# Performance work log

Hardware: AMD Instinct MI355X
Metric: run time of the kernel (lower is better)

The kernel has to match this reference:

```python
import jax, jax.numpy as jnp
import numpy as np

GRID_NUM = 5   # number of grid intervals (pykan default)
SPLINE_K = 3   # B-spline degree (pykan default)
GRID_RANGE = (-1.0, 1.0)


def make_grid(in_dim):
    # Extended uniform grid: num + 2k + 1 knots per input dim, shared values.
    h = (GRID_RANGE[1] - GRID_RANGE[0]) / GRID_NUM
    pts = GRID_RANGE[0] + h * jnp.arange(-SPLINE_K, GRID_NUM + SPLINE_K + 1, dtype=jnp.float32)
    return jnp.broadcast_to(pts, (in_dim, pts.shape[0]))  # (in_dim, num+2k+1)


def bspline_basis(x, grid, k):
    # Cox-de Boor recursion. x: (n, d); grid: (d, m). Returns (n, d, m-1-k).
    xe = x[..., None]            # (n, d, 1)
    g = grid[None]               # (1, d, m)
    B = ((xe >= g[..., :-1]) & (xe < g[..., 1:])).astype(x.dtype)
    for p in range(1, k + 1):
        left = (xe - g[..., :-(p + 1)]) / (g[..., p:-1] - g[..., :-(p + 1)])
        right = (g[..., p + 1:] - xe) / (g[..., p + 1:] - g[..., 1:-p])
        B = left * B[..., :-1] + right * B[..., 1:]
    return B


def kan_layer(x, coef, scale_base, scale_sp, grid):
    # x: (n, in); coef: (in, out, G+k); scales: (in, out)
    basis = bspline_basis(x, grid, SPLINE_K)              # (n, in, G+k)
    base = jax.nn.silu(x)                                 # (n, in)
    # y[n,o] = sum_i scale_base[i,o]*silu(x[n,i]) + scale_sp[i,o]*sum_g B[n,i,g]*coef[i,o,g]
    spline = jnp.einsum('nig,iog->no', basis, coef * scale_sp[:, :, None])
    return base @ scale_base + spline


def setup_inputs() -> dict:
    key = jax.random.key(0)
    ks = jax.random.split(key, 5)
    b, s, hid, ffn = 2, 4096, 512, 2048
    nb = GRID_NUM + SPLINE_K  # 8 basis functions
    x = jax.random.normal(ks[0], (b, s, hid), dtype=jnp.float32)
    coef1 = 0.1 * jax.random.normal(ks[1], (hid, ffn, nb), dtype=jnp.float32)
    scale_base1 = (1.0 / np.sqrt(hid)) * jax.random.normal(ks[2], (hid, ffn), dtype=jnp.float32)
    scale_sp1 = jnp.ones((hid, ffn), dtype=jnp.float32)
    coef2 = 0.1 * jax.random.normal(ks[3], (ffn, hid, nb), dtype=jnp.float32)
    scale_base2 = (1.0 / np.sqrt(ffn)) * jax.random.normal(ks[4], (ffn, hid), dtype=jnp.float32)
    scale_sp2 = jnp.ones((ffn, hid), dtype=jnp.float32)
    return {'x': x, 'coef1': coef1, 'scale_base1': scale_base1, 'scale_sp1': scale_sp1,
            'coef2': coef2, 'scale_base2': scale_base2, 'scale_sp2': scale_sp2}


def reference(x, coef1, scale_base1, scale_sp1, coef2, scale_base2, scale_sp2):
    b, s, hid = x.shape
    ffn = coef1.shape[1]
    grid1 = make_grid(hid)   # non-trainable buffers, derived from defaults
    grid2 = make_grid(ffn)
    h = x.reshape(b * s, hid)                     # rearrange 'b s h -> (b s) h'
    h = kan_layer(h, coef1, scale_base1, scale_sp1, grid1)
    h = kan_layer(h, coef2, scale_base2, scale_sp2, grid2)
    return h.reshape(b, s, hid)
```

## Files before the change

kernel.cpp:

```cpp
#include <hip/hip_runtime.h>
#include <cstdint>
#include <cstddef>

typedef _Float16 f16;
typedef _Float16 f16x8 __attribute__((ext_vector_type(8)));
typedef float f32x4 __attribute__((ext_vector_type(4)));


template <int I, int O>
__global__ void prep_coef(const float* __restrict__ coef,
                          const float* __restrict__ ssp,
                          f16* __restrict__ Wt) {
  constexpr int K32 = (9 * I) / 32;
  int tid = blockIdx.x * 256 + threadIdx.x;
  if (tid >= I * O) return;
  int i = tid / O, o = tid % O;
  float s = ssp[tid];
  const float* c = coef + (size_t)tid * 8;
  f16x8 out;
#pragma unroll
  for (int g = 0; g < 8; ++g) out[g] = (f16)(c[g] * s);
  size_t addr = ((size_t)(o >> 4) * K32 + (i >> 2)) * 512 +
                (size_t)(((i & 3) * 16) + (o & 15)) * 8;
  *(f16x8*)(Wt + addr) = out;
}

template <int I, int O>
__global__ void prep_base(const float* __restrict__ sb, f16* __restrict__ Wt) {
  constexpr int K32 = (9 * I) / 32;
  int tid = blockIdx.x * 256 + threadIdx.x;
  if (tid >= (I / 8) * O) return;
  int i8 = tid / O, o = tid % O;
  f16x8 out;
#pragma unroll
  for (int s = 0; s < 8; ++s)
    out[s] = (f16)sb[(size_t)(i8 * 8 + s) * O + o];
  size_t addr = ((size_t)(o >> 4) * K32 + (I / 4) + (i8 >> 2)) * 512 +
                (size_t)(((i8 & 3) * 16) + (o & 15)) * 8;
  *(f16x8*)(Wt + addr) = out;
}

__device__ __forceinline__ f16x8 spline8(float h) {
  float v = __builtin_fmaf(2.5f, h, 5.5f);
  float c = floorf(v);
  float f = v - c;
  float f2 = f * f, f3 = f2 * f;
  float b3 = f3 * (1.f / 6.f);
  float t = 1.f - f;
  float b0 = t * t * t * (1.f / 6.f);
  float b1 = (2.f / 3.f) - f2 + 0.5f * f3;
  float b2 = 1.f - b0 - b1 - b3;
  unsigned int u01 =
      __builtin_bit_cast(unsigned int, __builtin_amdgcn_cvt_pkrtz(b0, b1));
  unsigned int u23 =
      __builtin_bit_cast(unsigned int, __builtin_amdgcn_cvt_pkrtz(b2, b3));
  unsigned long long pk = (unsigned long long)u01 |
                          ((unsigned long long)u23 << 32);
  int ci = (int)c;
  int s = (ci - 3) * 16;
  __uint128_t r = 0;
  if (s >= 0) {
    if (s < 128) r = (__uint128_t)pk << s;
  } else {
    int q = -s;
    if (q < 64) r = (__uint128_t)(pk >> q);
  }
  return __builtin_bit_cast(f16x8, r);
}

template <int I, int ATOMIC>
__global__ __launch_bounds__(256, 2) void gemm_kan(const float* __restrict__ H,
                                                   const f16* __restrict__ W,
                                                   float* __restrict__ C,
                                                   int N, int kChunk) {
  constexpr int K = 9 * I;
  constexpr int KB = 8 * I;
  constexpr int K32 = K / 32;
  __shared__ __align__(16) f16 sA[2 * 128 * 64];
  const int t = threadIdx.x;
  const int n0 = blockIdx.x * 256;
  const int m0 = blockIdx.y * 128;
  const int kBeg = blockIdx.z * kChunk;
  const int kEnd = kBeg + kChunk;
  const int w = t >> 6, lane = t & 63;
  const int wm = (w >> 1) * 64, wn = (w & 1) * 128;
  const int lr = lane & 15, lq = lane >> 4;
  const int srow = t >> 3;
  const int j_ = t & 7;
  const int js = j_ ^ (srow & 7);

  f32x4 acc[4][8] = {};
  const float* Hrow = H + (size_t)(m0 + srow) * I;
  const f16* Pw = W + (size_t)((n0 + wn) >> 4) * K32 * 512 + lane * 8;

  float hs[4];

  auto genTile = [&](int kg, f16* wb) {
    if (kg < KB) {
#pragma unroll
      for (int q = 0; q < 4; ++q)
        *(f16x8*)&wb[((q * 32 + srow) * 8 + js) * 8] = spline8(hs[q]);
      const int kn = kg + 64;
      if (kn < kEnd && kn < KB) {
        const int i0n = kn >> 3;
#pragma unroll
        for (int q = 0; q < 4; ++q)
          hs[q] = Hrow[(size_t)(q * 32) * I + i0n + j_];
      }
    } else {
      const int c0 = (kg - KB) + j_ * 8;
      f32x4 ha[4][2];
#pragma unroll
      for (int q = 0; q < 4; ++q) {
        const f32x4* p = (const f32x4*)(Hrow + (size_t)(q * 32) * I + c0);
        ha[q][0] = p[0];
        ha[q][1] = p[1];
      }
#pragma unroll
      for (int q = 0; q < 4; ++q) {
        f16x8 o;
#pragma unroll
        for (int s = 0; s < 8; ++s) {
          float h = ha[q][s >> 2][s & 3];
          o[s] = (f16)(h / (1.f + __expf(-h)));
        }
        *(f16x8*)&wb[((q * 32 + srow) * 8 + js) * 8] = o;
      }
    }
  };

  if (kBeg < KB) {
    const int i0 = kBeg >> 3;
#pragma unroll
    for (int q = 0; q < 4; ++q)
      hs[q] = Hrow[(size_t)(q * 32) * I + i0 + j_];
  }
  genTile(kBeg, sA);
  __syncthreads();

  int cur = 0;
#pragma unroll 2
  for (int k0 = kBeg; k0 < kEnd; k0 += 64) {
    const int kb0 = k0 >> 5;
    const f16* rb = sA + cur * (128 * 64);
    f16* wb = sA + (cur ^ 1) * (128 * 64);

    f16x8 bv0[8];
#pragma unroll
    for (int j = 0; j < 8; ++j)
      bv0[j] = *(const f16x8*)(Pw + ((size_t)j * K32 + kb0) * 512);

    f16x8 av[4], bv1[8];
#pragma unroll
    for (int i = 0; i < 4; ++i) {
      const int ra = wm + i * 16 + lr;
      const int ca = lq ^ (ra & 7);
      av[i] = *(const f16x8*)&rb[ra * 64 + ca * 8];
    }
#pragma unroll
    for (int j = 0; j < 8; ++j)
      bv1[j] = *(const f16x8*)(Pw + ((size_t)j * K32 + kb0 + 1) * 512);

#pragma unroll
    for (int i = 0; i < 4; ++i)
#pragma unroll
      for (int j = 0; j < 8; ++j)
        acc[i][j] = __builtin_amdgcn_mfma_f32_16x16x32_f16(av[i], bv0[j],
                                                           acc[i][j], 0, 0, 0);

#pragma unroll
    for (int i = 0; i < 4; ++i) {
      const int ra = wm + i * 16 + lr;
      const int ca = (4 + lq) ^ (ra & 7);
      av[i] = *(const f16x8*)&rb[ra * 64 + ca * 8];
    }

    if (k0 + 64 < kEnd) genTile(k0 + 64, wb);

#pragma unroll
    for (int i = 0; i < 4; ++i)
#pragma unroll
      for (int j = 0; j < 8; ++j)
        acc[i][j] = __builtin_amdgcn_mfma_f32_16x16x32_f16(av[i], bv1[j],
                                                           acc[i][j], 0, 0, 0);

    __syncthreads();
    cur ^= 1;
  }

#pragma unroll
  for (int i = 0; i < 4; ++i) {
#pragma unroll
    for (int j = 0; j < 8; ++j) {
      const int col = n0 + wn + j * 16 + lr;
#pragma unroll
      for (int r = 0; r < 4; ++r) {
        const int row = m0 + wm + i * 16 + lq * 4 + r;
        if (ATOMIC)
          atomicAdd(&C[(size_t)row * N + col], acc[i][j][r]);
        else
          C[(size_t)row * N + col] = acc[i][j][r];
      }
    }
  }
}

extern "C" void kernel_launch(void* const* d_in, const int* in_sizes, int n_in,
                              void* d_out, int out_size, void* d_ws,
                              size_t ws_size, hipStream_t stream) {
  const float* x     = (const float*)d_in[0];
  const float* coef1 = (const float*)d_in[1];
  const float* sb1   = (const float*)d_in[2];
  const float* ssp1  = (const float*)d_in[3];
  const float* coef2 = (const float*)d_in[4];
  const float* sb2   = (const float*)d_in[5];
  const float* ssp2  = (const float*)d_in[6];

  const int Mtot = 8192;
  const int I1 = 512, O1 = 2048, K1 = I1 * 9;
  const int I2 = 2048, O2 = 512, K2 = I2 * 9;

  char* ws = (char*)d_ws;
  const size_t szW1 = (size_t)O1 * K1 * sizeof(f16);
  const size_t szW2 = (size_t)O2 * K2 * sizeof(f16);
  const size_t szH  = (size_t)Mtot * O1 * sizeof(float);
  if (ws_size < szW1 + szW2 + szH) return;
  f16*   W1 = (f16*)ws;
  f16*   W2 = (f16*)(ws + szW1);
  float* h1 = (float*)(ws + szW1 + szW2);

  {
    int n1 = I1 * O1;
    prep_coef<512, 2048><<<(n1 + 255) / 256, 256, 0, stream>>>(coef1, ssp1, W1);
    prep_base<512, 2048><<<(n1 / 8 + 255) / 256, 256, 0, stream>>>(sb1, W1);
    int n2 = I2 * O2;
    prep_coef<2048, 512><<<(n2 + 255) / 256, 256, 0, stream>>>(coef2, ssp2, W2);
    prep_base<2048, 512><<<(n2 / 8 + 255) / 256, 256, 0, stream>>>(sb2, W2);
  }

  gemm_kan<512, 0><<<dim3(O1 / 256, Mtot / 128, 1), 256, 0, stream>>>(
      x, W1, h1, O1, K1);

  (void)hipMemsetAsync(d_out, 0, (size_t)Mtot * O2 * sizeof(float), stream);
  const int SK = 4;
  gemm_kan<2048, 1><<<dim3(O2 / 256, Mtot / 128, SK), 256, 0, stream>>>(
      h1, W2, (float*)d_out, O2, K2 / SK);
}
```

Before: 518.3 us.

## Prefetch weight fragments across iterations, interleave split-K, swizzle block order, raise MFMA priority

The weight fragment loads are software-pipelined: the first half of the next step's B fragments is issued before tile generation, so global latency overlaps with spline/SiLU work and MFMAs. The grid is flattened to 1D so that groups of eight consecutive workgroups share the same row block, which is meant to improve L2 reuse of activations. Split-K for the second layer now interleaves 64-wide k-chunks across splits, which spreads the spline and SiLU segments evenly. s_setprio is raised around the MFMA bursts. The costs are higher register pressure from the extra prefetched fragments, and a hardcoded mapping that assumes exactly 8 workgroups per row group.

```diff
diff --git a/kernel.cpp b/kernel.cpp
--- a/kernel.cpp
+++ b/kernel.cpp
@@ -68,20 +68,23 @@
   return __builtin_bit_cast(f16x8, r);
 }
 
-template <int I, int ATOMIC>
+template <int I, int ATOMIC, int NX, int NZ>
 __global__ __launch_bounds__(256, 2) void gemm_kan(const float* __restrict__ H,
                                                    const f16* __restrict__ W,
                                                    float* __restrict__ C,
-                                                   int N, int kChunk) {
+                                                   int N) {
   constexpr int K = 9 * I;
   constexpr int KB = 8 * I;
   constexpr int K32 = K / 32;
+  constexpr int KSTEP = 64 * NZ;
+  constexpr int NSTEP = K / KSTEP;
   __shared__ __align__(16) f16 sA[2 * 128 * 64];
   const int t = threadIdx.x;
-  const int n0 = blockIdx.x * 256;
-  const int m0 = blockIdx.y * 128;
-  const int kBeg = blockIdx.z * kChunk;
-  const int kEnd = kBeg + kChunk;
+  const int wg = blockIdx.x;
+  const int pr = wg & 7;
+  const int n0 = (pr % NX) * 256;
+  const int m0 = (wg >> 3) * 128;
+  const int kBeg = (pr / NX) * 64;
   const int w = t >> 6, lane = t & 63;
   const int wm = (w >> 1) * 64, wn = (w & 1) * 128;
   const int lr = lane & 15, lq = lane >> 4;
@@ -91,7 +94,6 @@
 
   f32x4 acc[4][8] = {};
   const float* Hrow = H + (size_t)(m0 + srow) * I;
-  const f16* Pw = W + (size_t)((n0 + wn) >> 4) * K32 * 512 + lane * 8;
 
   float hs[4];
 
@@ -100,8 +102,8 @@
 #pragma unroll
       for (int q = 0; q < 4; ++q)
         *(f16x8*)&wb[((q * 32 + srow) * 8 + js) * 8] = spline8(hs[q]);
-      const int kn = kg + 64;
-      if (kn < kEnd && kn < KB) {
+      const int kn = kg + KSTEP;
+      if (kn < KB) {
         const int i0n = kn >> 3;
 #pragma unroll
         for (int q = 0; q < 4; ++q)
@@ -135,38 +137,41 @@
     for (int q = 0; q < 4; ++q)
       hs[q] = Hrow[(size_t)(q * 32) * I + i0 + j_];
   }
+  const f16* pk = W + ((size_t)((n0 + wn) >> 4) * K32 + (kBeg >> 5)) * 512 +
+                  lane * 8;
+  f16x8 bvA[8];
+#pragma unroll
+  for (int j = 0; j < 8; ++j)
+    bvA[j] = *(const f16x8*)(pk + (size_t)j * K32 * 512);
   genTile(kBeg, sA);
   __syncthreads();
 
   int cur = 0;
-#pragma unroll 2
-  for (int k0 = kBeg; k0 < kEnd; k0 += 64) {
-    const int kb0 = k0 >> 5;
+  for (int s = 0; s < NSTEP; ++s) {
     const f16* rb = sA + cur * (128 * 64);
     f16* wb = sA + (cur ^ 1) * (128 * 64);
 
-    f16x8 bv0[8];
+    f16x8 bvB[8];
 #pragma unroll
     for (int j = 0; j < 8; ++j)
-      bv0[j] = *(const f16x8*)(Pw + ((size_t)j * K32 + kb0) * 512);
-
-    f16x8 av[4], bv1[8];
+      bvB[j] = *(const f16x8*)(pk + (size_t)j * K32 * 512 + 512);
+
+    f16x8 av[4];
 #pragma unroll
     for (int i = 0; i < 4; ++i) {
       const int ra = wm + i * 16 + lr;
       const int ca = lq ^ (ra & 7);
       av[i] = *(const f16x8*)&rb[ra * 64 + ca * 8];
     }
-#pragma unroll
-    for (int j = 0; j < 8; ++j)
-      bv1[j] = *(const f16x8*)(Pw + ((size_t)j * K32 + kb0 + 1) * 512);
-
+
+    __builtin_amdgcn_s_setprio(1);
 #pragma unroll
     for (int i = 0; i < 4; ++i)
 #pragma unroll
       for (int j = 0; j < 8; ++j)
-        acc[i][j] = __builtin_amdgcn_mfma_f32_16x16x32_f16(av[i], bv0[j],
+        acc[i][j] = __builtin_amdgcn_mfma_f32_16x16x32_f16(av[i], bvA[j],
                                                            acc[i][j], 0, 0, 0);
+    __builtin_amdgcn_s_setprio(0);
 
 #pragma unroll
     for (int i = 0; i < 4; ++i) {
@@ -175,14 +180,24 @@
       av[i] = *(const f16x8*)&rb[ra * 64 + ca * 8];
     }
 
-    if (k0 + 64 < kEnd) genTile(k0 + 64, wb);
-
+    const bool more = (s + 1 < NSTEP);
+    if (more) genTile(kBeg + (s + 1) * KSTEP, wb);
+
+    pk += (size_t)(KSTEP / 32) * 512;
+    if (more) {
+#pragma unroll
+      for (int j = 0; j < 8; ++j)
+        bvA[j] = *(const f16x8*)(pk + (size_t)j * K32 * 512);
+    }
+
+    __builtin_amdgcn_s_setprio(1);
 #pragma unroll
     for (int i = 0; i < 4; ++i)
 #pragma unroll
       for (int j = 0; j < 8; ++j)
-        acc[i][j] = __builtin_amdgcn_mfma_f32_16x16x32_f16(av[i], bv1[j],
+        acc[i][j] = __builtin_amdgcn_mfma_f32_16x16x32_f16(av[i], bvB[j],
                                                            acc[i][j], 0, 0, 0);
+    __builtin_amdgcn_s_setprio(0);
 
     __syncthreads();
     cur ^= 1;
@@ -238,11 +253,9 @@
     prep_base<2048, 512><<<(n2 / 8 + 255) / 256, 256, 0, stream>>>(sb2, W2);
   }
 
-  gemm_kan<512, 0><<<dim3(O1 / 256, Mtot / 128, 1), 256, 0, stream>>>(
-      x, W1, h1, O1, K1);
+  gemm_kan<512, 0, 8, 1><<<dim3(512), 256, 0, stream>>>(x, W1, h1, O1);
 
   (void)hipMemsetAsync(d_out, 0, (size_t)Mtot * O2 * sizeof(float), stream);
-  const int SK = 4;
-  gemm_kan<2048, 1><<<dim3(O2 / 256, Mtot / 128, SK), 256, 0, stream>>>(
-      h1, W2, (float*)d_out, O2, K2 / SK);
-}
+  gemm_kan<2048, 1, 2, 4><<<dim3(512), 256, 0, stream>>>(h1, W2,
+                                                         (float*)d_out, O2);
+}
```

After: 500.2 us. -3.5%, faster.
